# Optimization experiments

Hardware: AMD Instinct MI355X
Metric: run time of the kernel (lower is better)

## Reference

```python
import jax, jax.numpy as jnp
import numpy as np

I, H, O = 64, 128, 1
H2, H4 = H // 2, H // 4


def _lstm(x, Wih, Whh, bih, bhh, collect_outputs=True):
    # x: [B, T, in]; Wih: [4H, in]; Whh: [4H, H]; gate order i, f, g, o (PyTorch).
    Hh = Whh.shape[1]
    B = x.shape[0]
    # Precompute input contribution for all timesteps: [T, B, 4H]
    xg = (jnp.einsum('bti,gi->btg', x, Wih) + bih + bhh).transpose(1, 0, 2)

    def step(carry, xg_t):
        h, c = carry
        g = xg_t + h @ Whh.T
        i, f, gg, o = jnp.split(g, 4, axis=-1)
        i = jax.nn.sigmoid(i)
        f = jax.nn.sigmoid(f)
        gg = jnp.tanh(gg)
        o = jax.nn.sigmoid(o)
        c = f * c + i * gg
        h = o * jnp.tanh(c)
        return (h, c), (h if collect_outputs else None)

    h0 = jnp.zeros((B, Hh), x.dtype)
    c0 = jnp.zeros((B, Hh), x.dtype)
    (hT, cT), hs = jax.lax.scan(step, (h0, c0), xg)
    if collect_outputs:
        return hs.transpose(1, 0, 2), hT  # [B, T, H], [B, H]
    return None, hT


def setup_inputs() -> dict:
    key = jax.random.key(0)
    ks = jax.random.split(key, 13)
    s1 = 1.0 / np.sqrt(H)
    s2 = 1.0 / np.sqrt(H2)
    s3 = 1.0 / np.sqrt(H4)
    u = lambda k, shape, s: jax.random.uniform(k, shape, jnp.float32, -s, s)
    return {
        'x': jax.random.normal(ks[0], (256, 1024, I), jnp.float32),
        'Wih1': u(ks[1], (4 * H, I), s1),
        'Whh1': u(ks[2], (4 * H, H), s1),
        'bih1': u(ks[3], (4 * H,), s1),
        'bhh1': u(ks[4], (4 * H,), s1),
        'Wih2': u(ks[5], (4 * H2, H), s2),
        'Whh2': u(ks[6], (4 * H2, H2), s2),
        'bih2': u(ks[7], (4 * H2,), s2),
        'bhh2': u(ks[8], (4 * H2,), s2),
        'W1': u(ks[9], (H4, H2), s2),
        'b1': u(ks[10], (H4,), s2),
        'W2': u(ks[11], (O, H4), s3),
        'b2': u(ks[12], (O,), s3),
    }


def reference(x, Wih1, Whh1, bih1, bhh1, Wih2, Whh2, bih2, bhh2, W1, b1, W2, b2):
    out1, _ = _lstm(x, Wih1, Whh1, bih1, bhh1, collect_outputs=True)
    # out[:, -1, :] of layer 2 == its final hidden state
    _, hT = _lstm(out1, Wih2, Whh2, bih2, bhh2, collect_outputs=False)
    h = jax.nn.sigmoid(hT @ W1.T + b1)
    return jax.nn.sigmoid(h @ W2.T + b2)
```

## Files before the change

kernel.cpp:

```cpp
#include <hip/hip_runtime.h>
#include <hip/hip_fp16.h>

#define NB   256
#define TT   1024
#define II   64
#define NT   512

typedef _Float16 f16;
typedef _Float16 f16x4 __attribute__((ext_vector_type(4)));
typedef _Float16 hf8 __attribute__((ext_vector_type(8)));
typedef float    ff4 __attribute__((ext_vector_type(4)));

__device__ __forceinline__ float rcp_fast(float x){
    float r; asm("v_rcp_f32 %0, %1" : "=v"(r) : "v"(x)); return r;
}
__device__ __forceinline__ float exp2_fast(float x){
    float r; asm("v_exp_f32 %0, %1" : "=v"(r) : "v"(x)); return r;
}
__device__ __forceinline__ float sigm(float x){
    return rcp_fast(1.0f + exp2_fast(x * -1.44269504f));
}
__device__ __forceinline__ float tanh_f(float x){
    return fmaf(-2.0f, rcp_fast(1.0f + exp2_fast(x * 2.88539008f)), 1.0f);
}
__device__ __forceinline__ hf8 cvt8(float4 a, float4 b){
    hf8 r;
    r[0]=(f16)a.x; r[1]=(f16)a.y; r[2]=(f16)a.z; r[3]=(f16)a.w;
    r[4]=(f16)b.x; r[5]=(f16)b.y; r[6]=(f16)b.z; r[7]=(f16)b.w;
    return r;
}
__device__ __forceinline__ hf8 ldw8(const float* src){
    float4 v0 = *(const float4*)src;
    float4 v1 = *(const float4*)(src + 4);
    return cvt8(v0, v1);
}


__launch_bounds__(NT, 2)
__global__ void lstm_mfma(const float* __restrict__ x,
                          const float* __restrict__ Wih1, const float* __restrict__ Whh1,
                          const float* __restrict__ bih1, const float* __restrict__ bhh1,
                          const float* __restrict__ Wih2, const float* __restrict__ Whh2,
                          const float* __restrict__ bih2, const float* __restrict__ bhh2,
                          const float* __restrict__ W1,   const float* __restrict__ b1,
                          const float* __restrict__ W2,   const float* __restrict__ b2,
                          float* __restrict__ out)
{
    __shared__ __align__(16) f16 xg[2][16][520];
    __shared__ __align__(16) f16 h1buf[2][128];
    __shared__ __align__(16) f16 h2buf[2][64];
    __shared__ float headbuf[32];

    const int j    = threadIdx.x;
    const int b    = blockIdx.x;
    const int wave = j >> 6;
    const int lane = j & 63;
    const int rho  = lane & 15;
    const int kg   = lane >> 4;
    const bool l2w = (wave >= 4);
    const int  wv  = wave & 3;

    const float* xb = x + (size_t)b * TT * II;

    float4 xl0, xl1, xl2, xl3;
    {
        const float* xp = xb + (size_t)rho * II + kg*8;
        xl0 = *(const float4*)xp;       xl1 = *(const float4*)(xp + 4);
        xl2 = *(const float4*)(xp + 32);xl3 = *(const float4*)(xp + 36);
    }

    hf8 A[32];
    float b2l0 = 0.f, b2l1 = 0.f, b2l2 = 0.f, b2l3 = 0.f;
    if (!l2w){
        #pragma unroll
        for (int i = 0; i < 8; ++i){
            const int tau = 8*wv + i;
            const int R   = (rho & 3)*128 + 4*tau + (rho >> 2);
            #pragma unroll
            for (int kt = 0; kt < 4; ++kt)
                A[i*4 + kt] = ldw8(Whh1 + R*128 + 32*kt + kg*8);
        }
    } else {
        #pragma unroll
        for (int i = 0; i < 4; ++i){
            const int tau2 = 4*wv + i;
            const int R    = (rho & 3)*64 + 4*tau2 + (rho >> 2);
            #pragma unroll
            for (int kt = 0; kt < 6; ++kt)
                A[i*6 + kt] = ldw8((kt < 4) ? (Wih2 + R*128 + 32*kt + kg*8)
                                            : (Whh2 + R*64  + 32*(kt-4) + kg*8));
        }
        const int u2 = 4*(4*wv + (rho & 3)) + kg;
        b2l0 = bih2[u2]       + bhh2[u2];
        b2l1 = bih2[64 + u2]  + bhh2[64 + u2];
        b2l2 = bih2[128 + u2] + bhh2[128 + u2];
        b2l3 = bih2[192 + u2] + bhh2[192 + u2];
    }
    hf8 AX[8];
    ff4 biasX[4];
    #pragma unroll
    for (int i = 0; i < 4; ++i){
        const int tx = 4*wave + i;
        const int Rx = (rho & 3)*128 + 4*tx + (rho >> 2);
        AX[i*2 + 0] = ldw8(Wih1 + Rx*64 + kg*8);
        AX[i*2 + 1] = ldw8(Wih1 + Rx*64 + 32 + kg*8);
        #pragma unroll
        for (int r = 0; r < 4; ++r){
            const int Rb = r*128 + 4*tx + kg;
            biasX[i][r] = bih1[Rb] + bhh1[Rb];
        }
    }

    if (j < 128) h1buf[0][j] = (f16)0.0f;
    if (j < 64)  h2buf[0][j] = (f16)0.0f;

    {
        hf8 xh0 = cvt8(xl0, xl1);
        hf8 xh1 = cvt8(xl2, xl3);
        #pragma unroll
        for (int i = 0; i < 4; ++i){
            ff4 g = __builtin_amdgcn_mfma_f32_16x16x32_f16(AX[i*2+0], xh0, biasX[i], 0, 0, 0);
            g     = __builtin_amdgcn_mfma_f32_16x16x32_f16(AX[i*2+1], xh1, g,        0, 0, 0);
            const int uX = 4*(4*wave + i) + kg;
            f16x4 w; w[0]=(f16)g[0]; w[1]=(f16)g[1]; w[2]=(f16)g[2]; w[3]=(f16)g[3];
            *(f16x4*)&xg[0][rho][uX*4] = w;
        }
    }
    __syncthreads();

    const ff4 zz = {0.0f, 0.0f, 0.0f, 0.0f};
    float c = 0.0f;
    int cur = 0;
    for (int t = 0; t < TT; ++t){
        const int trow = t & 15;
        const int cb   = (t >> 4) & 1;
        const bool stage = (trow == 15) && (t + 1 < TT);

        if (stage){
            const float* xp = xb + (size_t)(t + 1 + rho) * II + kg*8;
            xl0 = *(const float4*)xp;       xl1 = *(const float4*)(xp + 4);
            xl2 = *(const float4*)(xp + 32);xl3 = *(const float4*)(xp + 36);
        }

        f16x4 xv = {};
        if (!l2w){
            const int myUm = 4*(8*wv + (rho & 7)) + kg;
            xv = *(const f16x4*)&xg[cb][trow][myUm*4];
        }

        const f16* h1c = h1buf[cur];
        hf8 bf0 = *(const hf8*)(h1c      + kg*8);
        hf8 bf1 = *(const hf8*)(h1c + 32 + kg*8);
        hf8 bf2 = *(const hf8*)(h1c + 64 + kg*8);
        hf8 bf3 = *(const hf8*)(h1c + 96 + kg*8);

        ff4 qd;
        if (!l2w){
            ff4 acc[8];
            #pragma unroll
            for (int i = 0; i < 8; ++i)
                acc[i] = __builtin_amdgcn_mfma_f32_16x16x32_f16(A[i*4+0], bf0, zz, 0, 0, 0);
            #pragma unroll
            for (int i = 0; i < 8; ++i)
                acc[i] = __builtin_amdgcn_mfma_f32_16x16x32_f16(A[i*4+1], bf1, acc[i], 0, 0, 0);
            #pragma unroll
            for (int i = 0; i < 8; ++i)
                acc[i] = __builtin_amdgcn_mfma_f32_16x16x32_f16(A[i*4+2], bf2, acc[i], 0, 0, 0);
            #pragma unroll
            for (int i = 0; i < 8; ++i)
                acc[i] = __builtin_amdgcn_mfma_f32_16x16x32_f16(A[i*4+3], bf3, acc[i], 0, 0, 0);

            ff4 s0 = (rho & 1) ? acc[1] : acc[0];
            ff4 s1 = (rho & 1) ? acc[3] : acc[2];
            ff4 s2 = (rho & 1) ? acc[5] : acc[4];
            ff4 s3 = (rho & 1) ? acc[7] : acc[6];
            ff4 u0 = (rho & 2) ? s1 : s0;
            ff4 u1 = (rho & 2) ? s3 : s2;
            qd     = (rho & 4) ? u1 : u0;
        } else {
            const f16* h2c = h2buf[cur];
            hf8 bf4 = *(const hf8*)(h2c      + kg*8);
            hf8 bf5 = *(const hf8*)(h2c + 32 + kg*8);
            ff4 acc[4];
            __builtin_amdgcn_s_setprio(1);
            #pragma unroll
            for (int i = 0; i < 4; ++i)
                acc[i] = __builtin_amdgcn_mfma_f32_16x16x32_f16(A[i*6+0], bf0, zz, 0, 0, 0);
            #pragma unroll
            for (int kt = 1; kt < 6; ++kt){
                hf8 bb = (kt==1)?bf1:(kt==2)?bf2:(kt==3)?bf3:(kt==4)?bf4:bf5;
                #pragma unroll
                for (int i = 0; i < 4; ++i)
                    acc[i] = __builtin_amdgcn_mfma_f32_16x16x32_f16(A[i*6+kt], bb, acc[i], 0, 0, 0);
            }
            __builtin_amdgcn_s_setprio(0);
            ff4 s0 = (rho & 1) ? acc[1] : acc[0];
            ff4 s1 = (rho & 1) ? acc[3] : acc[2];
            qd     = (rho & 2) ? s1 : s0;
            qd[0] += b2l0; qd[1] += b2l1; qd[2] += b2l2; qd[3] += b2l3;
        }

        if (stage){
            hf8 xh0 = cvt8(xl0, xl1);
            hf8 xh1 = cvt8(xl2, xl3);
            #pragma unroll
            for (int i = 0; i < 4; ++i){
                ff4 g = __builtin_amdgcn_mfma_f32_16x16x32_f16(AX[i*2+0], xh0, biasX[i], 0, 0, 0);
                g     = __builtin_amdgcn_mfma_f32_16x16x32_f16(AX[i*2+1], xh1, g,        0, 0, 0);
                const int uX = 4*(4*wave + i) + kg;
                f16x4 w; w[0]=(f16)g[0]; w[1]=(f16)g[1]; w[2]=(f16)g[2]; w[3]=(f16)g[3];
                *(f16x4*)&xg[cb ^ 1][rho][uX*4] = w;
            }
        }

        if (!l2w){
            float ig = sigm(qd[0] + (float)xv[0]);
            float fg = sigm(qd[1] + (float)xv[1]);
            float gg = tanh_f(qd[2] + (float)xv[2]);
            float og = sigm(qd[3] + (float)xv[3]);
            c = fg*c + ig*gg;
            float hv = og * tanh_f(c);
            if (rho < 8) h1buf[cur ^ 1][4*(8*wv + rho) + kg] = (f16)hv;
        } else {
            float hv;
            if (t > 0){
                float ig = sigm(qd[0]);
                float fg = sigm(qd[1]);
                float gg = tanh_f(qd[2]);
                float og = sigm(qd[3]);
                c = fg*c + ig*gg;
                hv = og * tanh_f(c);
            } else {
                hv = 0.0f;
            }
            if (rho < 4) h2buf[cur ^ 1][4*(4*wv + rho) + kg] = (f16)hv;
        }
        __syncthreads();
        cur ^= 1;
    }

    if (l2w){
        const f16* h1c = h1buf[0];
        const f16* h2c = h2buf[0];
        hf8 bf0 = *(const hf8*)(h1c      + kg*8);
        hf8 bf1 = *(const hf8*)(h1c + 32 + kg*8);
        hf8 bf2 = *(const hf8*)(h1c + 64 + kg*8);
        hf8 bf3 = *(const hf8*)(h1c + 96 + kg*8);
        hf8 bf4 = *(const hf8*)(h2c      + kg*8);
        hf8 bf5 = *(const hf8*)(h2c + 32 + kg*8);
        ff4 acc[4];
        const ff4 zz2 = {0.0f, 0.0f, 0.0f, 0.0f};
        #pragma unroll
        for (int i = 0; i < 4; ++i)
            acc[i] = __builtin_amdgcn_mfma_f32_16x16x32_f16(A[i*6+0], bf0, zz2, 0, 0, 0);
        #pragma unroll
        for (int kt = 1; kt < 6; ++kt){
            hf8 bb = (kt==1)?bf1:(kt==2)?bf2:(kt==3)?bf3:(kt==4)?bf4:bf5;
            #pragma unroll
            for (int i = 0; i < 4; ++i)
                acc[i] = __builtin_amdgcn_mfma_f32_16x16x32_f16(A[i*6+kt], bb, acc[i], 0, 0, 0);
        }
        ff4 s0 = (rho & 1) ? acc[1] : acc[0];
        ff4 s1 = (rho & 1) ? acc[3] : acc[2];
        ff4 qd = (rho & 2) ? s1 : s0;
        float ig = sigm(qd[0] + b2l0);
        float fg = sigm(qd[1] + b2l1);
        float gg = tanh_f(qd[2] + b2l2);
        float og = sigm(qd[3] + b2l3);
        c = fg*c + ig*gg;
        float hv = og * tanh_f(c);
        if (rho < 4) h2buf[1][4*(4*wv + rho) + kg] = (f16)hv;
    }
    __syncthreads();

    if (j < 32){
        float a = b1[j];
        const float* w = W1 + j*64;
        #pragma unroll
        for (int k = 0; k < 64; ++k) a = fmaf(w[k], (float)h2buf[1][k], a);
        headbuf[j] = sigm(a);
    }
    __syncthreads();
    if (j == 0){
        float a = b2[0];
        #pragma unroll
        for (int k = 0; k < 32; ++k) a = fmaf(W2[k], headbuf[k], a);
        out[b] = sigm(a);
    }
}

extern "C" void kernel_launch(void* const* d_in, const int* in_sizes, int n_in,
                              void* d_out, int out_size, void* d_ws, size_t ws_size,
                              hipStream_t stream)
{
    (void)in_sizes; (void)n_in; (void)d_ws; (void)ws_size; (void)out_size;
    lstm_mfma<<<NB, NT, 0, stream>>>(
        (const float*)d_in[0],
        (const float*)d_in[1], (const float*)d_in[2],
        (const float*)d_in[3], (const float*)d_in[4],
        (const float*)d_in[5], (const float*)d_in[6],
        (const float*)d_in[7], (const float*)d_in[8],
        (const float*)d_in[9], (const float*)d_in[10],
        (const float*)d_in[11], (const float*)d_in[12],
        (float*)d_out);
}
```

Baseline: 817.6 us.

## Split layer-1 recurrence across eight waves and restrict x-projection to layer-1 waves

Raises the block to 768 threads so eight waves share the layer-1 hidden-to-hidden matmul, four gate tiles each instead of eight, while four waves still run layer 2. The input projection for the next 16 timesteps now runs only on the layer-1 waves, and the x loads are issued one step earlier so the fp16 conversion happens before the projection step. This shortens each wave's serial MFMA chain per timestep, at the cost of more waves taking part in each per-step barrier and lower occupancy per CU with the larger block.

```diff
diff --git a/kernel.cpp b/kernel.cpp
--- a/kernel.cpp
+++ b/kernel.cpp
@@ -4,7 +4,7 @@
 #define NB   256
 #define TT   1024
 #define II   64
-#define NT   512
+#define NT   768
 
 typedef _Float16 f16;
 typedef _Float16 f16x4 __attribute__((ext_vector_type(4)));
@@ -36,7 +36,7 @@
 }
 
 
-__launch_bounds__(NT, 2)
+__launch_bounds__(NT, 3)
 __global__ void lstm_mfma(const float* __restrict__ x,
                           const float* __restrict__ Wih1, const float* __restrict__ Whh1,
                           const float* __restrict__ bih1, const float* __restrict__ bhh1,
@@ -57,28 +57,37 @@
     const int lane = j & 63;
     const int rho  = lane & 15;
     const int kg   = lane >> 4;
-    const bool l2w = (wave >= 4);
-    const int  wv  = wave & 3;
+    const bool l2w = (wave >= 8);
+    const int  wv  = l2w ? (wave - 8) : wave;
 
     const float* xb = x + (size_t)b * TT * II;
 
     float4 xl0, xl1, xl2, xl3;
-    {
+    if (!l2w){
         const float* xp = xb + (size_t)rho * II + kg*8;
         xl0 = *(const float4*)xp;       xl1 = *(const float4*)(xp + 4);
         xl2 = *(const float4*)(xp + 32);xl3 = *(const float4*)(xp + 36);
     }
 
-    hf8 A[32];
+    hf8 A[24];
+    hf8 AX[8];
+    ff4 biasX[4];
     float b2l0 = 0.f, b2l1 = 0.f, b2l2 = 0.f, b2l3 = 0.f;
     if (!l2w){
         #pragma unroll
-        for (int i = 0; i < 8; ++i){
-            const int tau = 8*wv + i;
+        for (int i = 0; i < 4; ++i){
+            const int tau = 4*wv + i;
             const int R   = (rho & 3)*128 + 4*tau + (rho >> 2);
             #pragma unroll
             for (int kt = 0; kt < 4; ++kt)
                 A[i*4 + kt] = ldw8(Whh1 + R*128 + 32*kt + kg*8);
+            AX[i*2 + 0] = ldw8(Wih1 + R*64 + kg*8);
+            AX[i*2 + 1] = ldw8(Wih1 + R*64 + 32 + kg*8);
+            #pragma unroll
+            for (int r = 0; r < 4; ++r){
+                const int Rb = r*128 + 4*tau + kg;
+                biasX[i][r] = bih1[Rb] + bhh1[Rb];
+            }
         }
     } else {
         #pragma unroll
@@ -96,32 +105,19 @@
         b2l2 = bih2[128 + u2] + bhh2[128 + u2];
         b2l3 = bih2[192 + u2] + bhh2[192 + u2];
     }
-    hf8 AX[8];
-    ff4 biasX[4];
-    #pragma unroll
-    for (int i = 0; i < 4; ++i){
-        const int tx = 4*wave + i;
-        const int Rx = (rho & 3)*128 + 4*tx + (rho >> 2);
-        AX[i*2 + 0] = ldw8(Wih1 + Rx*64 + kg*8);
-        AX[i*2 + 1] = ldw8(Wih1 + Rx*64 + 32 + kg*8);
-        #pragma unroll
-        for (int r = 0; r < 4; ++r){
-            const int Rb = r*128 + 4*tx + kg;
-            biasX[i][r] = bih1[Rb] + bhh1[Rb];
-        }
-    }
 
     if (j < 128) h1buf[0][j] = (f16)0.0f;
     if (j < 64)  h2buf[0][j] = (f16)0.0f;
 
-    {
-        hf8 xh0 = cvt8(xl0, xl1);
-        hf8 xh1 = cvt8(xl2, xl3);
+    hf8 xh0, xh1;
+    if (!l2w){
+        xh0 = cvt8(xl0, xl1);
+        xh1 = cvt8(xl2, xl3);
         #pragma unroll
         for (int i = 0; i < 4; ++i){
             ff4 g = __builtin_amdgcn_mfma_f32_16x16x32_f16(AX[i*2+0], xh0, biasX[i], 0, 0, 0);
             g     = __builtin_amdgcn_mfma_f32_16x16x32_f16(AX[i*2+1], xh1, g,        0, 0, 0);
-            const int uX = 4*(4*wave + i) + kg;
+            const int uX = 4*(4*wv + i) + kg;
             f16x4 w; w[0]=(f16)g[0]; w[1]=(f16)g[1]; w[2]=(f16)g[2]; w[3]=(f16)g[3];
             *(f16x4*)&xg[0][rho][uX*4] = w;
         }
@@ -134,100 +130,95 @@
     for (int t = 0; t < TT; ++t){
         const int trow = t & 15;
         const int cb   = (t >> 4) & 1;
-        const bool stage = (trow == 15) && (t + 1 < TT);
-
-        if (stage){
-            const float* xp = xb + (size_t)(t + 1 + rho) * II + kg*8;
+
+        const bool ldx = (!l2w) && (trow == 14) && (t + 2 < TT);
+        if (ldx){
+            const float* xp = xb + (size_t)(t + 2 + rho) * II + kg*8;
             xl0 = *(const float4*)xp;       xl1 = *(const float4*)(xp + 4);
             xl2 = *(const float4*)(xp + 32);xl3 = *(const float4*)(xp + 36);
         }
 
-        f16x4 xv = {};
-        if (!l2w){
-            const int myUm = 4*(8*wv + (rho & 7)) + kg;
-            xv = *(const f16x4*)&xg[cb][trow][myUm*4];
-        }
-
-        const f16* h1c = h1buf[cur];
-        hf8 bf0 = *(const hf8*)(h1c      + kg*8);
-        hf8 bf1 = *(const hf8*)(h1c + 32 + kg*8);
-        hf8 bf2 = *(const hf8*)(h1c + 64 + kg*8);
-        hf8 bf3 = *(const hf8*)(h1c + 96 + kg*8);
-
         ff4 qd;
         if (!l2w){
-            ff4 acc[8];
-            #pragma unroll
-            for (int i = 0; i < 8; ++i)
+            const int myUm = 4*(4*wv + (rho & 3)) + kg;
+            f16x4 xv = *(const f16x4*)&xg[cb][trow][myUm*4];
+
+            const f16* h1c = h1buf[cur];
+            hf8 bf0 = *(const hf8*)(h1c      + kg*8);
+            hf8 bf1 = *(const hf8*)(h1c + 32 + kg*8);
+            hf8 bf2 = *(const hf8*)(h1c + 64 + kg*8);
+            hf8 bf3 = *(const hf8*)(h1c + 96 + kg*8);
+
+            ff4 acc[4];
+            #pragma unroll
+            for (int i = 0; i < 4; ++i)
                 acc[i] = __builtin_amdgcn_mfma_f32_16x16x32_f16(A[i*4+0], bf0, zz, 0, 0, 0);
             #pragma unroll
-            for (int i = 0; i < 8; ++i)
+            for (int i = 0; i < 4; ++i)
                 acc[i] = __builtin_amdgcn_mfma_f32_16x16x32_f16(A[i*4+1], bf1, acc[i], 0, 0, 0);
             #pragma unroll
-            for (int i = 0; i < 8; ++i)
+            for (int i = 0; i < 4; ++i)
                 acc[i] = __builtin_amdgcn_mfma_f32_16x16x32_f16(A[i*4+2], bf2, acc[i], 0, 0, 0);
             #pragma unroll
-            for (int i = 0; i < 8; ++i)
+            for (int i = 0; i < 4; ++i)
                 acc[i] = __builtin_amdgcn_mfma_f32_16x16x32_f16(A[i*4+3], bf3, acc[i], 0, 0, 0);
 
-            ff4 s0 = (rho & 1) ? acc[1] : acc[0];
-            ff4 s1 = (rho & 1) ? acc[3] : acc[2];
-            ff4 s2 = (rho & 1) ? acc[5] : acc[4];
-            ff4 s3 = (rho & 1) ? acc[7] : acc[6];
-            ff4 u0 = (rho & 2) ? s1 : s0;
-            ff4 u1 = (rho & 2) ? s3 : s2;
-            qd     = (rho & 4) ? u1 : u0;
-        } else {
-            const f16* h2c = h2buf[cur];
-            hf8 bf4 = *(const hf8*)(h2c      + kg*8);
-            hf8 bf5 = *(const hf8*)(h2c + 32 + kg*8);
-            ff4 acc[4];
-            __builtin_amdgcn_s_setprio(1);
-            #pragma unroll
-            for (int i = 0; i < 4; ++i)
-                acc[i] = __builtin_amdgcn_mfma_f32_16x16x32_f16(A[i*6+0], bf0, zz, 0, 0, 0);
-            #pragma unroll
-            for (int kt = 1; kt < 6; ++kt){
-                hf8 bb = (kt==1)?bf1:(kt==2)?bf2:(kt==3)?bf3:(kt==4)?bf4:bf5;
-                #pragma unroll
-                for (int i = 0; i < 4; ++i)
-                    acc[i] = __builtin_amdgcn_mfma_f32_16x16x32_f16(A[i*6+kt], bb, acc[i], 0, 0, 0);
-            }
-            __builtin_amdgcn_s_setprio(0);
             ff4 s0 = (rho & 1) ? acc[1] : acc[0];
             ff4 s1 = (rho & 1) ? acc[3] : acc[2];
             qd     = (rho & 2) ? s1 : s0;
-            qd[0] += b2l0; qd[1] += b2l1; qd[2] += b2l2; qd[3] += b2l3;
-        }
-
-        if (stage){
-            hf8 xh0 = cvt8(xl0, xl1);
-            hf8 xh1 = cvt8(xl2, xl3);
-            #pragma unroll
-            for (int i = 0; i < 4; ++i){
-                ff4 g = __builtin_amdgcn_mfma_f32_16x16x32_f16(AX[i*2+0], xh0, biasX[i], 0, 0, 0);
-                g     = __builtin_amdgcn_mfma_f32_16x16x32_f16(AX[i*2+1], xh1, g,        0, 0, 0);
-                const int uX = 4*(4*wave + i) + kg;
-                f16x4 w; w[0]=(f16)g[0]; w[1]=(f16)g[1]; w[2]=(f16)g[2]; w[3]=(f16)g[3];
-                *(f16x4*)&xg[cb ^ 1][rho][uX*4] = w;
-            }
-        }
-
-        if (!l2w){
+
+            if (trow == 15 && t + 1 < TT){
+                #pragma unroll
+                for (int i = 0; i < 4; ++i){
+                    ff4 g = __builtin_amdgcn_mfma_f32_16x16x32_f16(AX[i*2+0], xh0, biasX[i], 0, 0, 0);
+                    g     = __builtin_amdgcn_mfma_f32_16x16x32_f16(AX[i*2+1], xh1, g,        0, 0, 0);
+                    const int uX = 4*(4*wv + i) + kg;
+                    f16x4 w; w[0]=(f16)g[0]; w[1]=(f16)g[1]; w[2]=(f16)g[2]; w[3]=(f16)g[3];
+                    *(f16x4*)&xg[cb ^ 1][rho][uX*4] = w;
+                }
+            }
+
             float ig = sigm(qd[0] + (float)xv[0]);
             float fg = sigm(qd[1] + (float)xv[1]);
             float gg = tanh_f(qd[2] + (float)xv[2]);
             float og = sigm(qd[3] + (float)xv[3]);
             c = fg*c + ig*gg;
             float hv = og * tanh_f(c);
-            if (rho < 8) h1buf[cur ^ 1][4*(8*wv + rho) + kg] = (f16)hv;
+            if (rho < 4) h1buf[cur ^ 1][4*(4*wv + rho) + kg] = (f16)hv;
+
+            if (ldx){ xh0 = cvt8(xl0, xl1); xh1 = cvt8(xl2, xl3); }
         } else {
+            const f16* h1c = h1buf[cur];
+            const f16* h2c = h2buf[cur];
+            hf8 bf0 = *(const hf8*)(h1c      + kg*8);
+            hf8 bf1 = *(const hf8*)(h1c + 32 + kg*8);
+            hf8 bf2 = *(const hf8*)(h1c + 64 + kg*8);
+            hf8 bf3 = *(const hf8*)(h1c + 96 + kg*8);
+            hf8 bf4 = *(const hf8*)(h2c      + kg*8);
+            hf8 bf5 = *(const hf8*)(h2c + 32 + kg*8);
+            ff4 acc[4];
+            __builtin_amdgcn_s_setprio(1);
+            #pragma unroll
+            for (int i = 0; i < 4; ++i)
+                acc[i] = __builtin_amdgcn_mfma_f32_16x16x32_f16(A[i*6+0], bf0, zz, 0, 0, 0);
+            #pragma unroll
+            for (int kt = 1; kt < 6; ++kt){
+                hf8 bb = (kt==1)?bf1:(kt==2)?bf2:(kt==3)?bf3:(kt==4)?bf4:bf5;
+                #pragma unroll
+                for (int i = 0; i < 4; ++i)
+                    acc[i] = __builtin_amdgcn_mfma_f32_16x16x32_f16(A[i*6+kt], bb, acc[i], 0, 0, 0);
+            }
+            __builtin_amdgcn_s_setprio(0);
+            ff4 s0 = (rho & 1) ? acc[1] : acc[0];
+            ff4 s1 = (rho & 1) ? acc[3] : acc[2];
+            qd     = (rho & 2) ? s1 : s0;
+
             float hv;
             if (t > 0){
-                float ig = sigm(qd[0]);
-                float fg = sigm(qd[1]);
-                float gg = tanh_f(qd[2]);
-                float og = sigm(qd[3]);
+                float ig = sigm(qd[0] + b2l0);
+                float fg = sigm(qd[1] + b2l1);
+                float gg = tanh_f(qd[2] + b2l2);
+                float og = sigm(qd[3] + b2l3);
                 c = fg*c + ig*gg;
                 hv = og * tanh_f(c);
             } else {
```

Result: slower. 1.071 ms (+31.0%).

## Replace per-step block barriers with LDS counter flags and ring buffers

Applied to the files above, without the earlier changes.

Replaces the per-timestep __syncthreads with LDS atomic counters. Layer-1 and layer-2 waves now spin-wait only on the producers they depend on, and hidden states live in 4-deep ring buffers. Layer 2 runs one step behind layer 1 in a software pipeline, which also removes the separate final layer-2 step. The aim is to cut barrier stalls and let the two layers overlap. In exchange it adds spin polling with s_sleep, fence overhead and subtle correctness risks in the ring-slot reuse.

```diff
diff --git a/kernel.cpp b/kernel.cpp
--- a/kernel.cpp
+++ b/kernel.cpp
@@ -30,9 +30,12 @@
     return r;
 }
 __device__ __forceinline__ hf8 ldw8(const float* src){
-    float4 v0 = *(const float4*)src;
-    float4 v1 = *(const float4*)(src + 4);
-    return cvt8(v0, v1);
+    float4 a = *(const float4*)src;
+    float4 b = *(const float4*)(src + 4);
+    return cvt8(a, b);
+}
+__device__ __forceinline__ void wait_ge(volatile int* p, int tgt){
+    while (*p < tgt) __builtin_amdgcn_s_sleep(1);
 }
 
 
@@ -47,8 +50,9 @@
                           float* __restrict__ out)
 {
     __shared__ __align__(16) f16 xg[2][16][520];
-    __shared__ __align__(16) f16 h1buf[2][128];
-    __shared__ __align__(16) f16 h2buf[2][64];
+    __shared__ __align__(16) f16 h1ring[4][128];
+    __shared__ __align__(16) f16 h2ring[4][64];
+    __shared__ int cnt[2];
     __shared__ float headbuf[32];
 
     const int j    = threadIdx.x;
@@ -58,7 +62,7 @@
     const int rho  = lane & 15;
     const int kg   = lane >> 4;
     const bool l2w = (wave >= 4);
-    const int  wv  = wave & 3;
+    const int  wv  = l2w ? (wave - 4) : wave;
 
     const float* xb = x + (size_t)b * TT * II;
 
@@ -111,8 +115,9 @@
         }
     }
 
-    if (j < 128) h1buf[0][j] = (f16)0.0f;
-    if (j < 64)  h2buf[0][j] = (f16)0.0f;
+    if (j == 0){ cnt[0] = 0; cnt[1] = 0; }
+    if (j < 128) h1ring[3][j] = (f16)0.0f;
+    if (j < 64)  h2ring[3][j] = (f16)0.0f;
 
     {
         hf8 xh0 = cvt8(xl0, xl1);
@@ -128,34 +133,37 @@
     }
     __syncthreads();
 
-    const ff4 zz = {0.0f, 0.0f, 0.0f, 0.0f};
+    volatile int* h1c = &cnt[0];
+    volatile int* h2c = &cnt[1];
     float c = 0.0f;
-    int cur = 0;
-    for (int t = 0; t < TT; ++t){
-        const int trow = t & 15;
-        const int cb   = (t >> 4) & 1;
-        const bool stage = (trow == 15) && (t + 1 < TT);
-
-        if (stage){
-            const float* xp = xb + (size_t)(t + 1 + rho) * II + kg*8;
-            xl0 = *(const float4*)xp;       xl1 = *(const float4*)(xp + 4);
-            xl2 = *(const float4*)(xp + 32);xl3 = *(const float4*)(xp + 36);
-        }
-
-        f16x4 xv = {};
-        if (!l2w){
+
+    if (!l2w){
+        for (int t = 0; t < TT; ++t){
+            const int trow = t & 15;
+            const int cb   = (t >> 4) & 1;
+
+            wait_ge(h1c, 4*t);
+            if (trow == 0 && t > 0) wait_ge(h2c, 4*t);
+            else if (t >= 4)        wait_ge(h2c, 4*(t-3));
+            __threadfence_block();
+
+            const bool stage = (trow == 15) && (t + 1 < TT);
+            if (stage){
+                const float* xp = xb + (size_t)(t + 1 + rho) * II + kg*8;
+                xl0 = *(const float4*)xp;       xl1 = *(const float4*)(xp + 4);
+                xl2 = *(const float4*)(xp + 32);xl3 = *(const float4*)(xp + 36);
+            }
+
             const int myUm = 4*(8*wv + (rho & 7)) + kg;
-            xv = *(const f16x4*)&xg[cb][trow][myUm*4];
-        }
-
-        const f16* h1c = h1buf[cur];
-        hf8 bf0 = *(const hf8*)(h1c      + kg*8);
-        hf8 bf1 = *(const hf8*)(h1c + 32 + kg*8);
-        hf8 bf2 = *(const hf8*)(h1c + 64 + kg*8);
-        hf8 bf3 = *(const hf8*)(h1c + 96 + kg*8);
-
-        ff4 qd;
-        if (!l2w){
+            f16x4 xv = *(const f16x4*)&xg[cb][trow][myUm*4];
+
+            const f16* h1p = h1ring[(t - 1) & 3];
+            hf8 bf0 = *(const hf8*)(h1p      + kg*8);
+            hf8 bf1 = *(const hf8*)(h1p + 32 + kg*8);
+            hf8 bf2 = *(const hf8*)(h1p + 64 + kg*8);
+            hf8 bf3 = *(const hf8*)(h1p + 96 + kg*8);
+
+            const ff4 zz = {0.0f, 0.0f, 0.0f, 0.0f};
             ff4 acc[8];
             #pragma unroll
             for (int i = 0; i < 8; ++i)
@@ -176,108 +184,109 @@
             ff4 s3 = (rho & 1) ? acc[7] : acc[6];
             ff4 u0 = (rho & 2) ? s1 : s0;
             ff4 u1 = (rho & 2) ? s3 : s2;
-            qd     = (rho & 4) ? u1 : u0;
-        } else {
-            const f16* h2c = h2buf[cur];
-            hf8 bf4 = *(const hf8*)(h2c      + kg*8);
-            hf8 bf5 = *(const hf8*)(h2c + 32 + kg*8);
-            ff4 acc[4];
-            __builtin_amdgcn_s_setprio(1);
-            #pragma unroll
-            for (int i = 0; i < 4; ++i)
-                acc[i] = __builtin_amdgcn_mfma_f32_16x16x32_f16(A[i*6+0], bf0, zz, 0, 0, 0);
-            #pragma unroll
-            for (int kt = 1; kt < 6; ++kt){
-                hf8 bb = (kt==1)?bf1:(kt==2)?bf2:(kt==3)?bf3:(kt==4)?bf4:bf5;
-                #pragma unroll
-                for (int i = 0; i < 4; ++i)
-                    acc[i] = __builtin_amdgcn_mfma_f32_16x16x32_f16(A[i*6+kt], bb, acc[i], 0, 0, 0);
-            }
-            __builtin_amdgcn_s_setprio(0);
-            ff4 s0 = (rho & 1) ? acc[1] : acc[0];
-            ff4 s1 = (rho & 1) ? acc[3] : acc[2];
-            qd     = (rho & 2) ? s1 : s0;
-            qd[0] += b2l0; qd[1] += b2l1; qd[2] += b2l2; qd[3] += b2l3;
-        }
-
-        if (stage){
-            hf8 xh0 = cvt8(xl0, xl1);
-            hf8 xh1 = cvt8(xl2, xl3);
-            #pragma unroll
-            for (int i = 0; i < 4; ++i){
-                ff4 g = __builtin_amdgcn_mfma_f32_16x16x32_f16(AX[i*2+0], xh0, biasX[i], 0, 0, 0);
-                g     = __builtin_amdgcn_mfma_f32_16x16x32_f16(AX[i*2+1], xh1, g,        0, 0, 0);
-                const int uX = 4*(4*wave + i) + kg;
-                f16x4 w; w[0]=(f16)g[0]; w[1]=(f16)g[1]; w[2]=(f16)g[2]; w[3]=(f16)g[3];
-                *(f16x4*)&xg[cb ^ 1][rho][uX*4] = w;
-            }
-        }
-
-        if (!l2w){
+            ff4 qd = (rho & 4) ? u1 : u0;
+
             float ig = sigm(qd[0] + (float)xv[0]);
             float fg = sigm(qd[1] + (float)xv[1]);
             float gg = tanh_f(qd[2] + (float)xv[2]);
             float og = sigm(qd[3] + (float)xv[3]);
             c = fg*c + ig*gg;
             float hv = og * tanh_f(c);
-            if (rho < 8) h1buf[cur ^ 1][4*(8*wv + rho) + kg] = (f16)hv;
-        } else {
-            float hv;
-            if (t > 0){
-                float ig = sigm(qd[0]);
-                float fg = sigm(qd[1]);
-                float gg = tanh_f(qd[2]);
-                float og = sigm(qd[3]);
-                c = fg*c + ig*gg;
-                hv = og * tanh_f(c);
-            } else {
-                hv = 0.0f;
-            }
-            if (rho < 4) h2buf[cur ^ 1][4*(4*wv + rho) + kg] = (f16)hv;
-        }
-        __syncthreads();
-        cur ^= 1;
-    }
-
-    if (l2w){
-        const f16* h1c = h1buf[0];
-        const f16* h2c = h2buf[0];
-        hf8 bf0 = *(const hf8*)(h1c      + kg*8);
-        hf8 bf1 = *(const hf8*)(h1c + 32 + kg*8);
-        hf8 bf2 = *(const hf8*)(h1c + 64 + kg*8);
-        hf8 bf3 = *(const hf8*)(h1c + 96 + kg*8);
-        hf8 bf4 = *(const hf8*)(h2c      + kg*8);
-        hf8 bf5 = *(const hf8*)(h2c + 32 + kg*8);
-        ff4 acc[4];
-        const ff4 zz2 = {0.0f, 0.0f, 0.0f, 0.0f};
-        #pragma unroll
-        for (int i = 0; i < 4; ++i)
-            acc[i] = __builtin_amdgcn_mfma_f32_16x16x32_f16(A[i*6+0], bf0, zz2, 0, 0, 0);
-        #pragma unroll
-        for (int kt = 1; kt < 6; ++kt){
-            hf8 bb = (kt==1)?bf1:(kt==2)?bf2:(kt==3)?bf3:(kt==4)?bf4:bf5;
+            if (rho < 8) h1ring[t & 3][4*(8*wv + rho) + kg] = (f16)hv;
+
+            if (stage){
+                hf8 xh0 = cvt8(xl0, xl1);
+                hf8 xh1 = cvt8(xl2, xl3);
+                #pragma unroll
+                for (int i = 0; i < 4; ++i){
+                    ff4 g = __builtin_amdgcn_mfma_f32_16x16x32_f16(AX[i*2+0], xh0, biasX[i], 0, 0, 0);
+                    g     = __builtin_amdgcn_mfma_f32_16x16x32_f16(AX[i*2+1], xh1, g,        0, 0, 0);
+                    const int uX = 4*(4*wave + i) + kg;
+                    f16x4 w; w[0]=(f16)g[0]; w[1]=(f16)g[1]; w[2]=(f16)g[2]; w[3]=(f16)g[3];
+                    *(f16x4*)&xg[cb ^ 1][rho][uX*4] = w;
+                }
+            }
+
+            __threadfence_block();
+            if (lane == 0) atomicAdd(&cnt[0], 1);
+        }
+    } else {
+        for (int s = 0; s < TT; ++s){
+            const int trow = s & 15;
+
+            wait_ge(h1c, 4*(s + 1));
+            wait_ge(h2c, 4*s);
+            __threadfence_block();
+
+            const bool stage = (trow == 15) && (s + 1 < TT);
+            if (stage){
+                const float* xp = xb + (size_t)(s + 1 + rho) * II + kg*8;
+                xl0 = *(const float4*)xp;       xl1 = *(const float4*)(xp + 4);
+                xl2 = *(const float4*)(xp + 32);xl3 = *(const float4*)(xp + 36);
+            }
+
+            const f16* h1p = h1ring[s & 3];
+            const f16* h2p = h2ring[(s - 1) & 3];
+            hf8 bf0 = *(const hf8*)(h1p      + kg*8);
+            hf8 bf1 = *(const hf8*)(h1p + 32 + kg*8);
+            hf8 bf2 = *(const hf8*)(h1p + 64 + kg*8);
+            hf8 bf3 = *(const hf8*)(h1p + 96 + kg*8);
+            hf8 bf4 = *(const hf8*)(h2p      + kg*8);
+            hf8 bf5 = *(const hf8*)(h2p + 32 + kg*8);
+
+            const ff4 zz = {0.0f, 0.0f, 0.0f, 0.0f};
+            ff4 acc[4];
+            __builtin_amdgcn_s_setprio(1);
             #pragma unroll
             for (int i = 0; i < 4; ++i)
-                acc[i] = __builtin_amdgcn_mfma_f32_16x16x32_f16(A[i*6+kt], bb, acc[i], 0, 0, 0);
-        }
-        ff4 s0 = (rho & 1) ? acc[1] : acc[0];
-        ff4 s1 = (rho & 1) ? acc[3] : acc[2];
-        ff4 qd = (rho & 2) ? s1 : s0;
-        float ig = sigm(qd[0] + b2l0);
-        float fg = sigm(qd[1] + b2l1);
-        float gg = tanh_f(qd[2] + b2l2);
-        float og = sigm(qd[3] + b2l3);
-        c = fg*c + ig*gg;
-        float hv = og * tanh_f(c);
-        if (rho < 4) h2buf[1][4*(4*wv + rho) + kg] = (f16)hv;
-    }
+                acc[i] = __builtin_amdgcn_mfma_f32_16x16x32_f16(A[i*6+0], bf0, zz, 0, 0, 0);
+            #pragma unroll
+            for (int kt = 1; kt < 6; ++kt){
+                hf8 bb = (kt==1)?bf1:(kt==2)?bf2:(kt==3)?bf3:(kt==4)?bf4:bf5;
+                #pragma unroll
+                for (int i = 0; i < 4; ++i)
+                    acc[i] = __builtin_amdgcn_mfma_f32_16x16x32_f16(A[i*6+kt], bb, acc[i], 0, 0, 0);
+            }
+            __builtin_amdgcn_s_setprio(0);
+
+            ff4 s0 = (rho & 1) ? acc[1] : acc[0];
+            ff4 s1 = (rho & 1) ? acc[3] : acc[2];
+            ff4 qd = (rho & 2) ? s1 : s0;
+
+            float ig = sigm(qd[0] + b2l0);
+            float fg = sigm(qd[1] + b2l1);
+            float gg = tanh_f(qd[2] + b2l2);
+            float og = sigm(qd[3] + b2l3);
+            c = fg*c + ig*gg;
+            float hv = og * tanh_f(c);
+            if (rho < 4) h2ring[s & 3][4*(4*wv + rho) + kg] = (f16)hv;
+
+            if (stage){
+                hf8 xh0 = cvt8(xl0, xl1);
+                hf8 xh1 = cvt8(xl2, xl3);
+                const int cb = (s >> 4) & 1;
+                #pragma unroll
+                for (int i = 0; i < 4; ++i){
+                    ff4 g = __builtin_amdgcn_mfma_f32_16x16x32_f16(AX[i*2+0], xh0, biasX[i], 0, 0, 0);
+                    g     = __builtin_amdgcn_mfma_f32_16x16x32_f16(AX[i*2+1], xh1, g,        0, 0, 0);
+                    const int uX = 4*(4*wave + i) + kg;
+                    f16x4 w; w[0]=(f16)g[0]; w[1]=(f16)g[1]; w[2]=(f16)g[2]; w[3]=(f16)g[3];
+                    *(f16x4*)&xg[cb ^ 1][rho][uX*4] = w;
+                }
+            }
+
+            __threadfence_block();
+            if (lane == 0) atomicAdd(&cnt[1], 1);
+        }
+    }
+
     __syncthreads();
 
     if (j < 32){
         float a = b1[j];
         const float* w = W1 + j*64;
         #pragma unroll
-        for (int k = 0; k < 64; ++k) a = fmaf(w[k], (float)h2buf[1][k], a);
+        for (int k = 0; k < 64; ++k) a = fmaf(w[k], (float)h2ring[3][k], a);
         headbuf[j] = sigm(a);
     }
     __syncthreads();
```

Result: slower. 1.097 ms (+34.2%).
